# Kernel tuning notes

Hardware: AMD Instinct MI355X
Metric: run time of the kernel (lower is better)

Reference implementation:

```python
import jax, jax.numpy as jnp
import numpy as np

B, T, D_MODEL = 2, 2048, 2048
N_HEADS, N_KV_HEADS, HEAD_DIM = 16, 4, 128
N_REP = N_HEADS // N_KV_HEADS
EPS = 1e-6


def setup_inputs() -> dict:
    key = jax.random.key(0)
    ks = jax.random.split(key, 5)
    return {
        "x": jax.random.normal(ks[0], (B, T, D_MODEL), dtype=jnp.float32),
        "Wq": jax.random.normal(ks[1], (N_HEADS * HEAD_DIM, D_MODEL), dtype=jnp.float32) * 0.02,
        "Wk": jax.random.normal(ks[2], (N_KV_HEADS * HEAD_DIM, D_MODEL), dtype=jnp.float32) * 0.02,
        "Wv": jax.random.normal(ks[3], (N_KV_HEADS * HEAD_DIM, D_MODEL), dtype=jnp.float32) * 0.02,
        "Wo": jax.random.normal(ks[4], (D_MODEL, N_HEADS * HEAD_DIM), dtype=jnp.float32) * 0.02,
        "q_scale": jnp.ones((HEAD_DIM,), dtype=jnp.float32),
        "k_scale": jnp.ones((HEAD_DIM,), dtype=jnp.float32),
    }


def _qknorm(t, scale):
    # RMS-normalize along head_dim, then scale.
    norm = jax.lax.rsqrt(jnp.mean(t * t, axis=-1, keepdims=True) + EPS)
    return t * norm * scale


def reference(x, Wq, Wk, Wv, Wo, q_scale, k_scale):
    b, t, _ = x.shape
    # projections -> (B, H, T, D)
    q = (x @ Wq.T).reshape(b, t, N_HEADS, HEAD_DIM).transpose(0, 2, 1, 3)
    k = (x @ Wk.T).reshape(b, t, N_KV_HEADS, HEAD_DIM).transpose(0, 2, 1, 3)
    v = (x @ Wv.T).reshape(b, t, N_KV_HEADS, HEAD_DIM).transpose(0, 2, 1, 3)
    q = _qknorm(q, q_scale)
    k = _qknorm(k, k_scale)
    # GQA expansion: head h uses kv head h // n_rep
    k = jnp.repeat(k, N_REP, axis=1)
    v = jnp.repeat(v, N_REP, axis=1)
    # window_size (4096) >= seq_len, so no truncation occurs.
    scale = 1.0 / np.sqrt(HEAD_DIM).astype(np.float32)
    scores = jnp.einsum('bhtd,bhsd->bhts', q, k) * scale
    causal = jnp.tril(jnp.ones((t, t), dtype=bool))
    scores = jnp.where(causal, scores, jnp.finfo(scores.dtype).min)
    attn = jax.nn.softmax(scores, axis=-1)
    out = jnp.einsum('bhts,bhsd->bhtd', attn, v)
    out = out.transpose(0, 2, 1, 3).reshape(b, t, N_HEADS * HEAD_DIM)
    return out @ Wo.T
```

## Files before the change

### kernel.cpp

```cpp
#include <hip/hip_runtime.h>
#include <math.h>

#define Bn 2
#define Tn 2048
#define DM 2048
#define NH 16
#define NKV 4
#define HD 128

typedef __attribute__((ext_vector_type(8))) short bf16x8;
typedef __attribute__((ext_vector_type(4))) float f32x4;

__device__ __forceinline__ void cvt_split(float f, unsigned short& hi, unsigned short& lo) {
  union { float x; unsigned u; } a, b, c;
  a.x = f;
  hi = (unsigned short)(a.u >> 16);
  b.u = a.u & 0xFFFF0000u;
  c.x = f - b.x;
  lo = (unsigned short)(c.u >> 16);
}

#define BM 128
#define BNt 128
#define LROW 40

template <bool VT>
__device__ __forceinline__ void gemm_core(
    const float* __restrict__ A, const float* __restrict__ W,
    void* __restrict__ Cout, int m0, int n0, int ldC) {
  __shared__ unsigned short Ah[BM * LROW], Al[BM * LROW];
  __shared__ unsigned short Bh[BNt * LROW], Bl[BNt * LROW];

  const int tid = threadIdx.x;
  const int lane = tid & 63;
  const int w = tid >> 6;
  const int wr = w >> 1;
  const int wc = w & 1;
  const int g = lane >> 4;
  const int r16 = lane & 15;

  f32x4 acc[4][4];
#pragma unroll
  for (int i = 0; i < 4; ++i)
#pragma unroll
    for (int j = 0; j < 4; ++j) acc[i][j] = (f32x4){0.f, 0.f, 0.f, 0.f};

  for (int kk = 0; kk < DM; kk += 32) {
    float4 av[4], bv[4];
#pragma unroll
    for (int i = 0; i < 4; ++i) {
      const int idx = tid + 256 * i;
      const int row = idx >> 3;
      const int k4 = (idx & 7) << 2;
      av[i] = *(const float4*)&A[(size_t)(m0 + row) * DM + kk + k4];
      bv[i] = *(const float4*)&W[(size_t)(n0 + row) * DM + kk + k4];
    }
    __syncthreads();
#pragma unroll
    for (int i = 0; i < 4; ++i) {
      const int idx = tid + 256 * i;
      const int row = idx >> 3;
      const int s4 = (idx & 7) * 4;
      {
        unsigned short h0, l0, h1, l1, h2, l2, h3, l3;
        cvt_split(av[i].x, h0, l0); cvt_split(av[i].y, h1, l1);
        cvt_split(av[i].z, h2, l2); cvt_split(av[i].w, h3, l3);
        *(ushort4*)&Ah[row * LROW + s4] = make_ushort4(h0, h1, h2, h3);
        *(ushort4*)&Al[row * LROW + s4] = make_ushort4(l0, l1, l2, l3);
      }
      {
        unsigned short h0, l0, h1, l1, h2, l2, h3, l3;
        cvt_split(bv[i].x, h0, l0); cvt_split(bv[i].y, h1, l1);
        cvt_split(bv[i].z, h2, l2); cvt_split(bv[i].w, h3, l3);
        *(ushort4*)&Bh[row * LROW + s4] = make_ushort4(h0, h1, h2, h3);
        *(ushort4*)&Bl[row * LROW + s4] = make_ushort4(l0, l1, l2, l3);
      }
    }
    __syncthreads();

    bf16x8 ah[4], al[4];
#pragma unroll
    for (int mi = 0; mi < 4; ++mi) {
      const int ar = wr * 64 + mi * 16 + r16;
      ah[mi] = *(const bf16x8*)&Ah[ar * LROW + g * 8];
      al[mi] = *(const bf16x8*)&Al[ar * LROW + g * 8];
    }
#pragma unroll
    for (int ni = 0; ni < 4; ++ni) {
      const int brow = wc * 64 + ni * 16 + r16;
      bf16x8 bh = *(const bf16x8*)&Bh[brow * LROW + g * 8];
      bf16x8 bl = *(const bf16x8*)&Bl[brow * LROW + g * 8];
#pragma unroll
      for (int mi = 0; mi < 4; ++mi) {
        acc[mi][ni] = __builtin_amdgcn_mfma_f32_16x16x32_bf16(ah[mi], bh, acc[mi][ni], 0, 0, 0);
        acc[mi][ni] = __builtin_amdgcn_mfma_f32_16x16x32_bf16(ah[mi], bl, acc[mi][ni], 0, 0, 0);
        acc[mi][ni] = __builtin_amdgcn_mfma_f32_16x16x32_bf16(al[mi], bh, acc[mi][ni], 0, 0, 0);
      }
    }
  }

#pragma unroll
  for (int mi = 0; mi < 4; ++mi) {
#pragma unroll
    for (int r = 0; r < 4; ++r) {
      const int grow = m0 + wr * 64 + mi * 16 + g * 4 + r;
#pragma unroll
      for (int ni = 0; ni < 4; ++ni) {
        const int gcol = n0 + wc * 64 + ni * 16 + r16;
        const float val = acc[mi][ni][r];
        if constexpr (!VT) {
          ((float*)Cout)[(size_t)grow * ldC + gcol] = val;
        } else {
          const int bb = grow >> 11, t = grow & 2047;
          const int kvh = gcol >> 7, d = gcol & 127;
          unsigned short hi, lo;
          cvt_split(val, hi, lo);
          unsigned short* C = (unsigned short*)Cout;
          const size_t base = ((size_t)((bb * NKV + kvh) * 64 + (t >> 5))) * 8192;
          C[base + d * 32 + (t & 31)] = hi;
          C[base + 4096 + d * 32 + (t & 31)] = lo;
        }
      }
    }
  }
}

__global__ __launch_bounds__(256) void qkv_kernel(
    const float* __restrict__ x, const float* __restrict__ Wq,
    const float* __restrict__ Wk, const float* __restrict__ Wv,
    float* __restrict__ Qo, float* __restrict__ Ko, unsigned short* __restrict__ Vt) {
  const int bx = blockIdx.x;
  const int m0 = blockIdx.y * BM;
  if (bx < 16)      gemm_core<false>(x, Wq, Qo, m0, bx * 128, NH * HD);
  else if (bx < 20) gemm_core<false>(x, Wk, Ko, m0, (bx - 16) * 128, NKV * HD);
  else              gemm_core<true >(x, Wv, Vt, m0, (bx - 20) * 128, 0);
}

__global__ __launch_bounds__(256) void oproj_kernel(
    const float* __restrict__ O, const float* __restrict__ Wo,
    float* __restrict__ out) {
  gemm_core<false>(O, Wo, out, blockIdx.y * BM, blockIdx.x * BNt, DM);
}

__global__ __launch_bounds__(256) void rmsnorm_cvt_kernel(
    float* __restrict__ X, const float* __restrict__ scale) {
  const int row = blockIdx.x * 4 + (threadIdx.x >> 6);
  const int lane = threadIdx.x & 63;
  float2 v = *(const float2*)&X[(size_t)row * HD + lane * 2];
  float ss = fmaf(v.x, v.x, v.y * v.y);
#pragma unroll
  for (int off = 1; off < 64; off <<= 1) ss += __shfl_xor(ss, off);
  const float r = rsqrtf(ss * (1.0f / HD) + 1e-6f);
  float2 sc = *(const float2*)&scale[lane * 2];
  v.x *= r * sc.x;
  v.y *= r * sc.y;
  unsigned short h0, l0, h1, l1;
  cvt_split(v.x, h0, l0); cvt_split(v.y, h1, l1);
  unsigned short* rp = (unsigned short*)(X + (size_t)row * HD);
  *(ushort2*)&rp[lane * 2] = make_ushort2(h0, h1);
  *(ushort2*)&rp[128 + lane * 2] = make_ushort2(l0, l1);
}

#define AQT 64
#define AKT 32

__global__ __launch_bounds__(256) void attn_kernel(
    const unsigned short* __restrict__ Qus,
    const unsigned short* __restrict__ Kus,
    const unsigned short* __restrict__ Vt,
    float* __restrict__ Og) {
  __shared__ unsigned short Ksh[32 * 256];
  __shared__ unsigned short Vsh[2][128][40];
  __shared__ unsigned short Pws[4][2][16 * 40];

  const int bxp = blockIdx.x, h = blockIdx.y, b = blockIdx.z;
  const int kvh = h >> 2;
  const int tid = threadIdx.x;
  const int w = tid >> 6, lane = tid & 63;
  const int g = lane >> 4, r16 = lane & 15;
  const float sscale = 0.08838834764831845f;
  const int sw = (r16 & 7) << 4;
  const size_t vbase0 = (size_t)((b * NKV + kvh) * 64) * 8192;

  for (int ph = 0; ph < 2; ++ph) {
    const int qt = ph ? (31 - bxp) : bxp;
    const int q0 = qt * AQT;

    bf16x8 qh[4], ql[4];
    {
      const unsigned short* qrow =
          Qus + (size_t)(((b * Tn + q0 + w * 16 + r16) * NH) + h) * 256;
#pragma unroll
      for (int ks = 0; ks < 4; ++ks) {
        qh[ks] = *(const bf16x8*)(qrow + ks * 32 + g * 8);
        ql[ks] = *(const bf16x8*)(qrow + 128 + ks * 32 + g * 8);
      }
    }

    f32x4 o[8];
#pragma unroll
    for (int i = 0; i < 8; ++i) o[i] = (f32x4){0.f, 0.f, 0.f, 0.f};
    float m[4], l[4];
#pragma unroll
    for (int i = 0; i < 4; ++i) { m[i] = -INFINITY; l[i] = 0.f; }

    const int ntile = 2 * qt + 2;

    for (int kt = 0; kt < ntile; ++kt) {
      const int k0 = kt * AKT;
      bf16x8 kreg[4], vreg[4];
      int kj[4], kcho[4];
#pragma unroll
      for (int i = 0; i < 4; ++i) {
        int c = tid + 256 * i;
        kj[i] = c >> 5; kcho[i] = (c & 31) << 4;
        kreg[i] = *(const bf16x8*)(Kus +
            (size_t)(((b * Tn + k0 + kj[i]) * NKV) + kvh) * 256 + (kcho[i] >> 1));
        vreg[i] = *(const bf16x8*)(Vt + vbase0 + (size_t)kt * 8192 + (size_t)c * 8);
      }
      __syncthreads();
#pragma unroll
      for (int i = 0; i < 4; ++i) {
        int byte = (kj[i] << 9) + (kcho[i] ^ ((kj[i] & 7) << 4));
        *(bf16x8*)((char*)Ksh + byte) = kreg[i];
        int c = tid + 256 * i;
        int hl = c >> 9, cc = c & 511;
        *(bf16x8*)&Vsh[hl][cc >> 2][(cc & 3) * 8] = vreg[i];
      }
      __syncthreads();

      f32x4 s0 = (f32x4){0.f, 0.f, 0.f, 0.f};
      f32x4 s1 = (f32x4){0.f, 0.f, 0.f, 0.f};
      const char* Kb = (const char*)Ksh;
#pragma unroll
      for (int ks = 0; ks < 4; ++ks) {
        const int off = ks * 64 + g * 16;
        const int j0 = r16, j1 = 16 + r16;
        bf16x8 kh0 = *(const bf16x8*)(Kb + ((j0 << 9) + (off ^ sw)));
        bf16x8 kl0 = *(const bf16x8*)(Kb + ((j0 << 9) + ((256 + off) ^ sw)));
        bf16x8 kh1 = *(const bf16x8*)(Kb + ((j1 << 9) + (off ^ sw)));
        bf16x8 kl1 = *(const bf16x8*)(Kb + ((j1 << 9) + ((256 + off) ^ sw)));
        s0 = __builtin_amdgcn_mfma_f32_16x16x32_bf16(qh[ks], kh0, s0, 0, 0, 0);
        s0 = __builtin_amdgcn_mfma_f32_16x16x32_bf16(qh[ks], kl0, s0, 0, 0, 0);
        s0 = __builtin_amdgcn_mfma_f32_16x16x32_bf16(ql[ks], kh0, s0, 0, 0, 0);
        s1 = __builtin_amdgcn_mfma_f32_16x16x32_bf16(qh[ks], kh1, s1, 0, 0, 0);
        s1 = __builtin_amdgcn_mfma_f32_16x16x32_bf16(qh[ks], kl1, s1, 0, 0, 0);
        s1 = __builtin_amdgcn_mfma_f32_16x16x32_bf16(ql[ks], kh1, s1, 0, 0, 0);
      }

      float mloc[4];
#pragma unroll
      for (int rr = 0; rr < 4; ++rr) {
        const int qg = q0 + w * 16 + g * 4 + rr;
        float a0 = (k0 + r16 <= qg) ? s0[rr] * sscale : -INFINITY;
        float a1 = (k0 + 16 + r16 <= qg) ? s1[rr] * sscale : -INFINITY;
        s0[rr] = a0; s1[rr] = a1;
        mloc[rr] = fmaxf(a0, a1);
      }
#pragma unroll
      for (int off = 1; off < 16; off <<= 1)
#pragma unroll
        for (int rr = 0; rr < 4; ++rr) mloc[rr] = fmaxf(mloc[rr], __shfl_xor(mloc[rr], off));
      float alpha[4], lsum[4];
#pragma unroll
      for (int rr = 0; rr < 4; ++rr) {
        const float mnew = fmaxf(m[rr], mloc[rr]);
        alpha[rr] = __expf(m[rr] - mnew);
        m[rr] = mnew;
        const float p0 = __expf(s0[rr] - mnew);
        const float p1 = __expf(s1[rr] - mnew);
        s0[rr] = p0; s1[rr] = p1;
        lsum[rr] = p0 + p1;
      }
#pragma unroll
      for (int off = 1; off < 16; off <<= 1)
#pragma unroll
        for (int rr = 0; rr < 4; ++rr) lsum[rr] += __shfl_xor(lsum[rr], off);
#pragma unroll
      for (int rr = 0; rr < 4; ++rr) l[rr] = l[rr] * alpha[rr] + lsum[rr];
#pragma unroll
      for (int dt = 0; dt < 8; ++dt)
#pragma unroll
        for (int rr = 0; rr < 4; ++rr) o[dt][rr] *= alpha[rr];

#pragma unroll
      for (int rr = 0; rr < 4; ++rr) {
        const int q = g * 4 + rr;
        unsigned short hh, ll;
        cvt_split(s0[rr], hh, ll);
        Pws[w][0][q * 40 + r16] = hh; Pws[w][1][q * 40 + r16] = ll;
        cvt_split(s1[rr], hh, ll);
        Pws[w][0][q * 40 + 16 + r16] = hh; Pws[w][1][q * 40 + 16 + r16] = ll;
      }

      bf16x8 pah = *(const bf16x8*)&Pws[w][0][r16 * 40 + g * 8];
      bf16x8 pal = *(const bf16x8*)&Pws[w][1][r16 * 40 + g * 8];
#pragma unroll
      for (int dt = 0; dt < 8; ++dt) {
        const int d = dt * 16 + r16;
        bf16x8 vh = *(const bf16x8*)&Vsh[0][d][g * 8];
        bf16x8 vl = *(const bf16x8*)&Vsh[1][d][g * 8];
        o[dt] = __builtin_amdgcn_mfma_f32_16x16x32_bf16(pah, vh, o[dt], 0, 0, 0);
        o[dt] = __builtin_amdgcn_mfma_f32_16x16x32_bf16(pah, vl, o[dt], 0, 0, 0);
        o[dt] = __builtin_amdgcn_mfma_f32_16x16x32_bf16(pal, vh, o[dt], 0, 0, 0);
      }
    }

    float inv[4];
#pragma unroll
    for (int rr = 0; rr < 4; ++rr) inv[rr] = 1.f / l[rr];
#pragma unroll
    for (int dt = 0; dt < 8; ++dt)
#pragma unroll
      for (int rr = 0; rr < 4; ++rr) {
        Og[(size_t)(b * Tn + q0 + w * 16 + g * 4 + rr) * (NH * HD) + h * HD + dt * 16 + r16] =
            o[dt][rr] * inv[rr];
      }
  }
}

extern "C" void kernel_launch(void* const* d_in, const int* in_sizes, int n_in,
                              void* d_out, int out_size, void* d_ws, size_t ws_size,
                              hipStream_t stream) {
  const float* x = (const float*)d_in[0];
  const float* Wq = (const float*)d_in[1];
  const float* Wk = (const float*)d_in[2];
  const float* Wv = (const float*)d_in[3];
  const float* Wo = (const float*)d_in[4];
  const float* q_scale = (const float*)d_in[5];
  const float* k_scale = (const float*)d_in[6];
  float* out = (float*)d_out;

  const int R = Bn * Tn;
  float* Q = (float*)d_ws;
  float* K = Q + (size_t)R * (NH * HD);
  unsigned short* Vt = (unsigned short*)(K + (size_t)R * (NKV * HD));
  float* O = (float*)(Vt + (size_t)Bn * NKV * 64 * 8192);

  dim3 blk(256);
  qkv_kernel<<<dim3(24, R / BM), blk, 0, stream>>>(x, Wq, Wk, Wv, Q, K, Vt);
  rmsnorm_cvt_kernel<<<dim3(R * NH / 4), blk, 0, stream>>>(Q, q_scale);
  rmsnorm_cvt_kernel<<<dim3(R * NKV / 4), blk, 0, stream>>>(K, k_scale);
  attn_kernel<<<dim3(16, NH, Bn), blk, 0, stream>>>(
      (const unsigned short*)Q, (const unsigned short*)K, Vt, O);
  oproj_kernel<<<dim3(DM / BNt, R / BM), blk, 0, stream>>>(O, Wo, out);
}
```

Baseline: 651.1 us.

## Pre-split weights to bf16 hi/lo and load tiles via direct global-to-LDS

Adds a split kernel that converts each weight matrix into bf16 hi/lo halves once per call, so the GEMMs no longer split weights inside every tile. B tiles (and the attention output in the o-projection) are now loaded with global_load_lds 16-byte copies straight into shared memory, whose rows are unpadded at 32 elements. The attention kernel writes its output already split into hi/lo bf16. This removes repeated per-tile conversion ALU work and register staging, at the cost of extra split launches and workspace traffic, plus possible LDS bank conflicts from dropping the padding.

```diff
diff --git a/kernel.cpp b/kernel.cpp
--- a/kernel.cpp
+++ b/kernel.cpp
@@ -20,24 +20,44 @@
   lo = (unsigned short)(c.u >> 16);
 }
 
-#define BM 128
-#define BNt 128
-#define LROW 40
-
-template <bool VT>
+__device__ __forceinline__ void gload16(const unsigned short* g, unsigned short* l) {
+  __builtin_amdgcn_global_load_lds(
+      (const __attribute__((address_space(1))) void*)g,
+      (__attribute__((address_space(3))) void*)l, 16, 0, 0);
+}
+
+__global__ __launch_bounds__(256) void split_kernel(
+    const float* __restrict__ src, unsigned short* __restrict__ h,
+    unsigned short* __restrict__ l, int n4) {
+  int i = blockIdx.x * 256 + threadIdx.x;
+  const int stride = gridDim.x * 256;
+  for (; i < n4; i += stride) {
+    float4 v = ((const float4*)src)[i];
+    ushort4 hh, ll;
+    cvt_split(v.x, hh.x, ll.x); cvt_split(v.y, hh.y, ll.y);
+    cvt_split(v.z, hh.z, ll.z); cvt_split(v.w, hh.w, ll.w);
+    ((ushort4*)h)[i] = hh;
+    ((ushort4*)l)[i] = ll;
+  }
+}
+
+template <bool APRE, bool VT>
 __device__ __forceinline__ void gemm_core(
-    const float* __restrict__ A, const float* __restrict__ W,
+    const float* __restrict__ Af,
+    const unsigned short* __restrict__ Agh, const unsigned short* __restrict__ Agl,
+    const unsigned short* __restrict__ Bgh, const unsigned short* __restrict__ Bgl,
     void* __restrict__ Cout, int m0, int n0, int ldC) {
-  __shared__ unsigned short Ah[BM * LROW], Al[BM * LROW];
-  __shared__ unsigned short Bh[BNt * LROW], Bl[BNt * LROW];
+  __shared__ unsigned short lA[2][128 * 32];
+  __shared__ unsigned short lB[2][128 * 32];
 
   const int tid = threadIdx.x;
   const int lane = tid & 63;
   const int w = tid >> 6;
-  const int wr = w >> 1;
-  const int wc = w & 1;
-  const int g = lane >> 4;
-  const int r16 = lane & 15;
+  const int wr = w >> 1, wc = w & 1;
+  const int g = lane >> 4, r16 = lane & 15;
+  const int lrow = lane >> 2;
+  const int lch = (lane & 3) * 8;
+  const int b0 = w * 32, b1 = w * 32 + 16;
 
   f32x4 acc[4][4];
 #pragma unroll
@@ -46,34 +66,37 @@
     for (int j = 0; j < 4; ++j) acc[i][j] = (f32x4){0.f, 0.f, 0.f, 0.f};
 
   for (int kk = 0; kk < DM; kk += 32) {
-    float4 av[4], bv[4];
-#pragma unroll
-    for (int i = 0; i < 4; ++i) {
-      const int idx = tid + 256 * i;
-      const int row = idx >> 3;
-      const int k4 = (idx & 7) << 2;
-      av[i] = *(const float4*)&A[(size_t)(m0 + row) * DM + kk + k4];
-      bv[i] = *(const float4*)&W[(size_t)(n0 + row) * DM + kk + k4];
+    float4 av[4];
+    if constexpr (!APRE) {
+#pragma unroll
+      for (int i = 0; i < 4; ++i) {
+        const int idx = tid + 256 * i;
+        const int row = idx >> 3;
+        const int k4 = (idx & 7) << 2;
+        av[i] = *(const float4*)&Af[(size_t)(m0 + row) * DM + kk + k4];
+      }
     }
     __syncthreads();
-#pragma unroll
-    for (int i = 0; i < 4; ++i) {
-      const int idx = tid + 256 * i;
-      const int row = idx >> 3;
-      const int s4 = (idx & 7) * 4;
-      {
+    gload16(&Bgh[(size_t)(n0 + b0 + lrow) * DM + kk + lch], &lB[0][b0 * 32]);
+    gload16(&Bgh[(size_t)(n0 + b1 + lrow) * DM + kk + lch], &lB[0][b1 * 32]);
+    gload16(&Bgl[(size_t)(n0 + b0 + lrow) * DM + kk + lch], &lB[1][b0 * 32]);
+    gload16(&Bgl[(size_t)(n0 + b1 + lrow) * DM + kk + lch], &lB[1][b1 * 32]);
+    if constexpr (APRE) {
+      gload16(&Agh[(size_t)(m0 + b0 + lrow) * DM + kk + lch], &lA[0][b0 * 32]);
+      gload16(&Agh[(size_t)(m0 + b1 + lrow) * DM + kk + lch], &lA[0][b1 * 32]);
+      gload16(&Agl[(size_t)(m0 + b0 + lrow) * DM + kk + lch], &lA[1][b0 * 32]);
+      gload16(&Agl[(size_t)(m0 + b1 + lrow) * DM + kk + lch], &lA[1][b1 * 32]);
+    } else {
+#pragma unroll
+      for (int i = 0; i < 4; ++i) {
+        const int idx = tid + 256 * i;
+        const int row = idx >> 3;
+        const int s4 = (idx & 7) * 4;
         unsigned short h0, l0, h1, l1, h2, l2, h3, l3;
         cvt_split(av[i].x, h0, l0); cvt_split(av[i].y, h1, l1);
         cvt_split(av[i].z, h2, l2); cvt_split(av[i].w, h3, l3);
-        *(ushort4*)&Ah[row * LROW + s4] = make_ushort4(h0, h1, h2, h3);
-        *(ushort4*)&Al[row * LROW + s4] = make_ushort4(l0, l1, l2, l3);
-      }
-      {
-        unsigned short h0, l0, h1, l1, h2, l2, h3, l3;
-        cvt_split(bv[i].x, h0, l0); cvt_split(bv[i].y, h1, l1);
-        cvt_split(bv[i].z, h2, l2); cvt_split(bv[i].w, h3, l3);
-        *(ushort4*)&Bh[row * LROW + s4] = make_ushort4(h0, h1, h2, h3);
-        *(ushort4*)&Bl[row * LROW + s4] = make_ushort4(l0, l1, l2, l3);
+        *(ushort4*)&lA[0][row * 32 + s4] = make_ushort4(h0, h1, h2, h3);
+        *(ushort4*)&lA[1][row * 32 + s4] = make_ushort4(l0, l1, l2, l3);
       }
     }
     __syncthreads();
@@ -82,14 +105,14 @@
 #pragma unroll
     for (int mi = 0; mi < 4; ++mi) {
       const int ar = wr * 64 + mi * 16 + r16;
-      ah[mi] = *(const bf16x8*)&Ah[ar * LROW + g * 8];
-      al[mi] = *(const bf16x8*)&Al[ar * LROW + g * 8];
+      ah[mi] = *(const bf16x8*)&lA[0][ar * 32 + g * 8];
+      al[mi] = *(const bf16x8*)&lA[1][ar * 32 + g * 8];
     }
 #pragma unroll
     for (int ni = 0; ni < 4; ++ni) {
       const int brow = wc * 64 + ni * 16 + r16;
-      bf16x8 bh = *(const bf16x8*)&Bh[brow * LROW + g * 8];
-      bf16x8 bl = *(const bf16x8*)&Bl[brow * LROW + g * 8];
+      bf16x8 bh = *(const bf16x8*)&lB[0][brow * 32 + g * 8];
+      bf16x8 bl = *(const bf16x8*)&lB[1][brow * 32 + g * 8];
 #pragma unroll
       for (int mi = 0; mi < 4; ++mi) {
         acc[mi][ni] = __builtin_amdgcn_mfma_f32_16x16x32_bf16(ah[mi], bh, acc[mi][ni], 0, 0, 0);
@@ -126,20 +149,23 @@
 }
 
 __global__ __launch_bounds__(256) void qkv_kernel(
-    const float* __restrict__ x, const float* __restrict__ Wq,
-    const float* __restrict__ Wk, const float* __restrict__ Wv,
+    const float* __restrict__ x,
+    const unsigned short* __restrict__ Wqh, const unsigned short* __restrict__ Wql,
+    const unsigned short* __restrict__ Wkh, const unsigned short* __restrict__ Wkl,
+    const unsigned short* __restrict__ Wvh, const unsigned short* __restrict__ Wvl,
     float* __restrict__ Qo, float* __restrict__ Ko, unsigned short* __restrict__ Vt) {
   const int bx = blockIdx.x;
-  const int m0 = blockIdx.y * BM;
-  if (bx < 16)      gemm_core<false>(x, Wq, Qo, m0, bx * 128, NH * HD);
-  else if (bx < 20) gemm_core<false>(x, Wk, Ko, m0, (bx - 16) * 128, NKV * HD);
-  else              gemm_core<true >(x, Wv, Vt, m0, (bx - 20) * 128, 0);
+  const int m0 = blockIdx.y * 128;
+  if (bx < 16)      gemm_core<false, false>(x, nullptr, nullptr, Wqh, Wql, Qo, m0, bx * 128, NH * HD);
+  else if (bx < 20) gemm_core<false, false>(x, nullptr, nullptr, Wkh, Wkl, Ko, m0, (bx - 16) * 128, NKV * HD);
+  else              gemm_core<false, true >(x, nullptr, nullptr, Wvh, Wvl, Vt, m0, (bx - 20) * 128, 0);
 }
 
 __global__ __launch_bounds__(256) void oproj_kernel(
-    const float* __restrict__ O, const float* __restrict__ Wo,
+    const unsigned short* __restrict__ Oh, const unsigned short* __restrict__ Ol,
+    const unsigned short* __restrict__ Woh, const unsigned short* __restrict__ Wol,
     float* __restrict__ out) {
-  gemm_core<false>(O, Wo, out, blockIdx.y * BM, blockIdx.x * BNt, DM);
+  gemm_core<true, false>(nullptr, Oh, Ol, Woh, Wol, out, blockIdx.y * 128, blockIdx.x * 128, DM);
 }
 
 __global__ __launch_bounds__(256) void rmsnorm_cvt_kernel(
@@ -168,7 +194,7 @@
     const unsigned short* __restrict__ Qus,
     const unsigned short* __restrict__ Kus,
     const unsigned short* __restrict__ Vt,
-    float* __restrict__ Og) {
+    unsigned short* __restrict__ Oh, unsigned short* __restrict__ Ol) {
   __shared__ unsigned short Ksh[32 * 256];
   __shared__ unsigned short Vsh[2][128][40];
   __shared__ unsigned short Pws[4][2][16 * 40];
@@ -313,8 +339,12 @@
     for (int dt = 0; dt < 8; ++dt)
 #pragma unroll
       for (int rr = 0; rr < 4; ++rr) {
-        Og[(size_t)(b * Tn + q0 + w * 16 + g * 4 + rr) * (NH * HD) + h * HD + dt * 16 + r16] =
-            o[dt][rr] * inv[rr];
+        const size_t oidx =
+            (size_t)(b * Tn + q0 + w * 16 + g * 4 + rr) * (NH * HD) + h * HD + dt * 16 + r16;
+        unsigned short hi, lo;
+        cvt_split(o[dt][rr] * inv[rr], hi, lo);
+        Oh[oidx] = hi;
+        Ol[oidx] = lo;
       }
   }
 }
@@ -332,16 +362,30 @@
   float* out = (float*)d_out;
 
   const int R = Bn * Tn;
-  float* Q = (float*)d_ws;
+  unsigned short* p = (unsigned short*)d_ws;
+  unsigned short* Wqh = p; p += (size_t)2048 * 2048;
+  unsigned short* Wql = p; p += (size_t)2048 * 2048;
+  unsigned short* Wkh = p; p += (size_t)512 * 2048;
+  unsigned short* Wkl = p; p += (size_t)512 * 2048;
+  unsigned short* Wvh = p; p += (size_t)512 * 2048;
+  unsigned short* Wvl = p; p += (size_t)512 * 2048;
+  unsigned short* Woh = p; p += (size_t)2048 * 2048;
+  unsigned short* Wol = p; p += (size_t)2048 * 2048;
+  unsigned short* Oh = p; p += (size_t)R * 2048;
+  unsigned short* Ol = p; p += (size_t)R * 2048;
+  unsigned short* Vt = p; p += (size_t)Bn * NKV * 64 * 8192;
+  float* Q = (float*)p;
   float* K = Q + (size_t)R * (NH * HD);
-  unsigned short* Vt = (unsigned short*)(K + (size_t)R * (NKV * HD));
-  float* O = (float*)(Vt + (size_t)Bn * NKV * 64 * 8192);
 
   dim3 blk(256);
-  qkv_kernel<<<dim3(24, R / BM), blk, 0, stream>>>(x, Wq, Wk, Wv, Q, K, Vt);
+  split_kernel<<<dim3(2048), blk, 0, stream>>>(Wq, Wqh, Wql, 2048 * 2048 / 4);
+  split_kernel<<<dim3(1024), blk, 0, stream>>>(Wk, Wkh, Wkl, 512 * 2048 / 4);
+  split_kernel<<<dim3(1024), blk, 0, stream>>>(Wv, Wvh, Wvl, 512 * 2048 / 4);
+  split_kernel<<<dim3(2048), blk, 0, stream>>>(Wo, Woh, Wol, 2048 * 2048 / 4);
+  qkv_kernel<<<dim3(24, R / 128), blk, 0, stream>>>(x, Wqh, Wql, Wkh, Wkl, Wvh, Wvl, Q, K, Vt);
   rmsnorm_cvt_kernel<<<dim3(R * NH / 4), blk, 0, stream>>>(Q, q_scale);
   rmsnorm_cvt_kernel<<<dim3(R * NKV / 4), blk, 0, stream>>>(K, k_scale);
   attn_kernel<<<dim3(16, NH, Bn), blk, 0, stream>>>(
-      (const unsigned short*)Q, (const unsigned short*)K, Vt, O);
-  oproj_kernel<<<dim3(DM / BNt, R / BM), blk, 0, stream>>>(O, Wo, out);
-}
+      (const unsigned short*)Q, (const unsigned short*)K, Vt, Oh, Ol);
+  oproj_kernel<<<dim3(DM / 128, R / 128), blk, 0, stream>>>(Oh, Ol, Woh, Wol, out);
+}
```

New measurement: 633.0 us. 1.03x faster.
